# Kernel optimization log

Hardware: AMD Instinct MI355X
Metric: run time of the kernel (lower is better)

The kernel has to match this reference:

```python
import jax, jax.numpy as jnp
import numpy as np

LN_EPS = 1e-5
NORM_EPS = 1e-12


def entmax15_last(x):
    """Exact 1.5-entmax over the last axis (Peters & Martins sort algorithm)."""
    d = x.shape[-1]
    x = x / 2.0
    x = x - jnp.max(x, axis=-1, keepdims=True)
    xs = jnp.sort(x, axis=-1)[..., ::-1]  # descending
    k = jnp.arange(1, d + 1, dtype=x.dtype)
    mean = jnp.cumsum(xs, axis=-1) / k
    meansq = jnp.cumsum(xs * xs, axis=-1) / k
    ss = k * (meansq - jnp.square(mean))
    delta = (1.0 - ss) / k
    tau = mean - jnp.sqrt(jnp.clip(delta, 0.0))
    support = (tau <= xs).astype(jnp.int32)
    k_star = jnp.sum(support, axis=-1, keepdims=True) - 1  # last valid index
    tau_star = jnp.take_along_axis(tau, k_star, axis=-1)
    return jnp.square(jnp.maximum(x - tau_star, 0.0))


def layer_norm(x, gamma, beta):
    mu = jnp.mean(x, axis=-1, keepdims=True)
    var = jnp.mean(jnp.square(x - mu), axis=-1, keepdims=True)
    return (x - mu) / jnp.sqrt(var + LN_EPS) * gamma + beta


def setup_inputs() -> dict:
    key = jax.random.key(0)
    ks = jax.random.split(key, 4)
    B, M, N, D, T, L = 256, 64, 32, 128, 64, 128
    return {
        "x": jax.random.normal(ks[0], (B, M, D), dtype=jnp.float32),
        "route_weights": jax.random.normal(ks[1], (M, N, D, T), dtype=jnp.float32),
        "thread": jax.random.uniform(ks[2], (1, M, N), dtype=jnp.float32),
        "routing_leaves": jax.random.uniform(ks[3], (L, T), dtype=jnp.float32),
        "ln_gamma": jnp.ones((T,), dtype=jnp.float32),
        "ln_beta": jnp.zeros((T,), dtype=jnp.float32),
    }


def reference(x, route_weights, thread, routing_leaves, ln_gamma, ln_beta):
    # entmax15 over dim=-2 (the in_capsule_size axis D) of route_weights [M,N,D,T]
    w = jnp.swapaxes(route_weights, -1, -2)
    w = entmax15_last(w)
    weights = jnp.swapaxes(w, -1, -2)
    # priors: [B, M, N, T]
    priors = jnp.einsum('bmd,mndt->bmnt', x, weights)
    # routing
    leave_hash = routing_leaves / jnp.maximum(
        jnp.linalg.norm(routing_leaves, axis=-1, keepdims=True), NORM_EPS)
    votes = jax.nn.sigmoid(jnp.einsum('ld,bmnt->bmnl', leave_hash, priors)) if False else \
        jax.nn.sigmoid(jnp.einsum('ld,bmnd->bmnl', leave_hash, priors))  # [B,M,N,L]
    mean_cap = jnp.mean(votes, axis=1, keepdims=True)
    dis = jnp.mean(jnp.square(votes - mean_cap), axis=-1)  # [B,M,N]
    weight = jax.nn.relu(jnp.square(thread) - dis)
    prob = jax.nn.softmax(weight, axis=-2)  # over M (in capsules)
    next_caps = jnp.sum(prob[:, :, :, None] * priors, axis=1)  # [B,N,T]
    return layer_norm(next_caps, ln_gamma, ln_beta)
```

## Files before the change

### kernel.cpp

```cpp
#include <hip/hip_runtime.h>
#include <hip/hip_bf16.h>
#include <math.h>

#define B_ 256
#define M_ 64
#define N_ 32
#define D_ 128
#define T_ 64
#define L_ 128

typedef __attribute__((ext_vector_type(8))) short short8;
typedef __attribute__((ext_vector_type(4))) float floatx4;

__device__ __forceinline__ unsigned short f2bf(float f) {
  unsigned int u = __float_as_uint(f);
  unsigned int r = (u + 0x7fffu + ((u >> 16) & 1u)) >> 16;
  return (unsigned short)r;
}
__device__ __forceinline__ float bf2f(unsigned short s) {
  return __uint_as_float(((unsigned int)s) << 16);
}
__device__ __forceinline__ float frcp(float x) { return __builtin_amdgcn_rcpf(x); }

__global__ __launch_bounds__(256) void k_entmax(const float* __restrict__ rw,
                                                unsigned short* __restrict__ wq2,
                                                const float* __restrict__ x,
                                                const float* __restrict__ leaves,
                                                unsigned short* __restrict__ xb2,
                                                unsigned short* __restrict__ lhn,
                                                const float* __restrict__ thr,
                                                float* __restrict__ thrT) {
  const int tid = threadIdx.x;
  const int bx = blockIdx.x;
  if (bx >= 1024) {
    int bid = bx - 1024;
    if (bid < 512) {
      int idx = bid * 256 + tid;
      int j = idx & 7, b = (idx >> 3) & 255, m = idx >> 11;
      const float* xs = x + ((size_t)b * M_ + m) * D_ + j;
      unsigned short pv[16];
#pragma unroll
      for (int i = 0; i < 16; ++i) pv[i] = f2bf(xs[i * 8]);
      unsigned short* dst = xb2 + ((size_t)m * B_ + b) * D_ + j * 16;
      uint4 w0, w1;
      w0.x = pv[0] | ((unsigned)pv[1] << 16);  w0.y = pv[2] | ((unsigned)pv[3] << 16);
      w0.z = pv[4] | ((unsigned)pv[5] << 16);  w0.w = pv[6] | ((unsigned)pv[7] << 16);
      w1.x = pv[8] | ((unsigned)pv[9] << 16);  w1.y = pv[10] | ((unsigned)pv[11] << 16);
      w1.z = pv[12] | ((unsigned)pv[13] << 16); w1.w = pv[14] | ((unsigned)pv[15] << 16);
      *(uint4*)(dst) = w0;
      *(uint4*)(dst + 8) = w1;
    } else if (bid == 512) {
      if (tid < L_) {
        const float* r = leaves + tid * T_;
        float ss = 0.f;
        for (int i = 0; i < T_; ++i) ss = fmaf(r[i], r[i], ss);
        float inv = frcp(fmaxf(sqrtf(ss), 1e-12f));
        unsigned short* o = lhn + tid * T_;
        for (int i = 0; i < T_; ++i) o[i] = f2bf(r[i] * inv);
      }
    } else {
#pragma unroll
      for (int k = 0; k < 8; ++k) {
        int idx = k * 256 + tid;
        int nn = idx >> 6, mm = idx & 63;
        thrT[idx] = thr[mm * N_ + nn];
      }
    }
    return;
  }

  const int mn = bx * 2 + (tid >> 7);
  const int sub = tid & 127;
  const int g = sub >> 3;
  const int j = sub & 7;
  const float* base = rw + (size_t)mn * D_ * T_ + g * 4;

  floatx4 xv[16];
#pragma unroll
  for (int i = 0; i < 16; ++i)
    xv[i] = *(const floatx4*)(base + (size_t)(i * 8 + j) * T_);

  floatx4 mx = xv[0];
#pragma unroll
  for (int i = 1; i < 16; ++i)
#pragma unroll
    for (int c = 0; c < 4; ++c) mx[c] = fmaxf(mx[c], xv[i][c]);
#pragma unroll
  for (int off = 1; off <= 4; off <<= 1)
#pragma unroll
    for (int c = 0; c < 4; ++c) mx[c] = fmaxf(mx[c], __shfl_xor(mx[c], off));
#pragma unroll
  for (int i = 0; i < 16; ++i)
#pragma unroll
    for (int c = 0; c < 4; ++c) xv[i][c] = (xv[i][c] - mx[c]) * 0.5f;

  floatx4 lo = (floatx4){-1.f, -1.f, -1.f, -1.f};
  floatx4 hi = (floatx4){0.f, 0.f, 0.f, 0.f};
  for (int it = 0; it < 10; ++it) {
    floatx4 tau, f = (floatx4){0.f, 0.f, 0.f, 0.f};
#pragma unroll
    for (int c = 0; c < 4; ++c) tau[c] = 0.5f * (lo[c] + hi[c]);
#pragma unroll
    for (int i = 0; i < 16; ++i)
#pragma unroll
      for (int c = 0; c < 4; ++c) {
        float u = fmaxf(xv[i][c] - tau[c], 0.0f);
        f[c] = fmaf(u, u, f[c]);
      }
#pragma unroll
    for (int off = 1; off <= 4; off <<= 1)
#pragma unroll
      for (int c = 0; c < 4; ++c) f[c] += __shfl_xor(f[c], off);
#pragma unroll
    for (int c = 0; c < 4; ++c) {
      bool ge = f[c] >= 1.0f;
      lo[c] = ge ? tau[c] : lo[c];
      hi[c] = ge ? hi[c] : tau[c];
    }
  }
  floatx4 tau0, cnt = (floatx4){0,0,0,0}, s1 = (floatx4){0,0,0,0}, s2 = (floatx4){0,0,0,0};
#pragma unroll
  for (int c = 0; c < 4; ++c) tau0[c] = 0.5f * (lo[c] + hi[c]);
#pragma unroll
  for (int i = 0; i < 16; ++i)
#pragma unroll
    for (int c = 0; c < 4; ++c) {
      bool in = xv[i][c] > tau0[c];
      float q = in ? xv[i][c] : 0.0f;
      cnt[c] += in ? 1.0f : 0.0f;
      s1[c] += q;
      s2[c] = fmaf(q, q, s2[c]);
    }
#pragma unroll
  for (int off = 1; off <= 4; off <<= 1)
#pragma unroll
    for (int c = 0; c < 4; ++c) {
      cnt[c] += __shfl_xor(cnt[c], off);
      s1[c] += __shfl_xor(s1[c], off);
      s2[c] += __shfl_xor(s2[c], off);
    }
  floatx4 tau;
#pragma unroll
  for (int c = 0; c < 4; ++c) {
    float rc = frcp(cnt[c]);
    float mean = s1[c] * rc;
    float ss = s2[c] - mean * s1[c];
    float delta = (1.0f - ss) * rc;
    tau[c] = mean - sqrtf(fmaxf(delta, 0.0f));
  }

#pragma unroll
  for (int c = 0; c < 4; ++c) {
    unsigned short pv[16];
#pragma unroll
    for (int i = 0; i < 16; ++i) {
      float u = fmaxf(xv[i][c] - tau[c], 0.0f);
      pv[i] = f2bf(u * u);
    }
    unsigned short* dst = wq2 + ((size_t)mn * 64 + g * 4 + c) * D_ + j * 16;
    uint4 w0, w1;
    w0.x = pv[0] | ((unsigned)pv[1] << 16);  w0.y = pv[2] | ((unsigned)pv[3] << 16);
    w0.z = pv[4] | ((unsigned)pv[5] << 16);  w0.w = pv[6] | ((unsigned)pv[7] << 16);
    w1.x = pv[8] | ((unsigned)pv[9] << 16);  w1.y = pv[10] | ((unsigned)pv[11] << 16);
    w1.z = pv[12] | ((unsigned)pv[13] << 16); w1.w = pv[14] | ((unsigned)pv[15] << 16);
    *(uint4*)(dst) = w0;
    *(uint4*)(dst + 8) = w1;
  }
}

#define BS_STRIDE 136
__global__ __launch_bounds__(256, 4) void k_priors(const unsigned short* __restrict__ xb2,
                                                   const unsigned short* __restrict__ wq2,
                                                   unsigned short* __restrict__ priors) {
  const int n = blockIdx.x, m = blockIdx.y;
  const int tid = threadIdx.x;
  const int wid = tid >> 6, lane = tid & 63;
  const int row16 = lane & 15, quad = lane >> 4;
  __shared__ __align__(16) unsigned short Bs[64 * BS_STRIDE];
  __shared__ __align__(16) unsigned short Ct[128 * 72];

  short8 xfr[2][2][4];
#pragma unroll
  for (int c = 0; c < 2; ++c)
#pragma unroll
    for (int sub = 0; sub < 2; ++sub) {
      const int b = c * 128 + wid * 32 + sub * 16 + row16;
      const unsigned short* xptr = xb2 + ((size_t)m * B_ + b) * D_ + quad * 8;
#pragma unroll
      for (int ks = 0; ks < 4; ++ks) xfr[c][sub][ks] = *(const short8*)(xptr + ks * 32);
    }

  {
    const unsigned short* bsrc = wq2 + ((size_t)(m * N_ + n) * T_) * D_;
    int tr = tid >> 4, cc = tid & 15;
#pragma unroll
    for (int p = 0; p < 4; ++p) {
      int row = p * 16 + tr;
      uint4 v = *(const uint4*)(bsrc + row * D_ + cc * 8);
      *(uint4*)&Bs[row * BS_STRIDE + cc * 8] = v;
    }
  }
  __syncthreads();

#pragma unroll
  for (int c = 0; c < 2; ++c) {
    floatx4 acc[2][4];
#pragma unroll
    for (int sub = 0; sub < 2; ++sub)
#pragma unroll
      for (int cf = 0; cf < 4; ++cf) acc[sub][cf] = (floatx4){0.f, 0.f, 0.f, 0.f};

#pragma unroll
    for (int cf = 0; cf < 4; ++cf) {
      short8 afr[4];
#pragma unroll
      for (int ks = 0; ks < 4; ++ks)
        afr[ks] = *(const short8*)&Bs[(cf * 16 + row16) * BS_STRIDE + ks * 32 + quad * 8];
#pragma unroll
      for (int ks = 0; ks < 4; ++ks)
#pragma unroll
        for (int sub = 0; sub < 2; ++sub)
          acc[sub][cf] = __builtin_amdgcn_mfma_f32_16x16x32_bf16(afr[ks], xfr[c][sub][ks], acc[sub][cf], 0, 0, 0);
    }

    if (c) __syncthreads();
#pragma unroll
    for (int sub = 0; sub < 2; ++sub)
#pragma unroll
      for (int cf = 0; cf < 4; ++cf) {
        ushort4 o4;
        o4.x = f2bf(acc[sub][cf][0]); o4.y = f2bf(acc[sub][cf][1]);
        o4.z = f2bf(acc[sub][cf][2]); o4.w = f2bf(acc[sub][cf][3]);
        *(ushort4*)&Ct[(wid * 32 + sub * 16 + row16) * 72 + cf * 16 + quad * 4] = o4;
      }
    __syncthreads();

    {
      int q = tid >> 4, s = tid & 15;
      int row = q * 8 + (s >> 1);
      int half = s & 1;
      int b = c * 128 + row;
      const unsigned short* src = &Ct[row * 72 + half * 32];
      unsigned short* dst = priors + (((size_t)n * B_ + b) * M_ + m) * T_ + half * 32;
      uint4 a0 = *(const uint4*)(src);
      uint4 a1 = *(const uint4*)(src + 8);
      uint4 a2 = *(const uint4*)(src + 16);
      uint4 a3 = *(const uint4*)(src + 24);
      *(uint4*)(dst) = a0;
      *(uint4*)(dst + 8) = a1;
      *(uint4*)(dst + 16) = a2;
      *(uint4*)(dst + 24) = a3;
    }
  }
}

__global__ __launch_bounds__(256, 4) void k_route(const unsigned short* __restrict__ priors,
                                                  const unsigned short* __restrict__ lhn,
                                                  const float* __restrict__ thrT,
                                                  const float* __restrict__ gamma,
                                                  const float* __restrict__ beta,
                                                  float* __restrict__ out) {
  const int n = blockIdx.x, g4 = blockIdx.y;
  const int tid = threadIdx.x;
  const int wid = tid >> 6, lane = tid & 63;
  const int col = lane & 15, quad = lane >> 4;

  __shared__ float probL[4][64];

  const int b = g4 * 4 + wid;

  const unsigned short* base = priors + ((size_t)n * B_ + b) * (M_ * T_);
  short8 afr[4][2];
#pragma unroll
  for (int mt = 0; mt < 4; ++mt)
#pragma unroll
    for (int ks = 0; ks < 2; ++ks)
      afr[mt][ks] = *(const short8*)(base + (mt * 16 + col) * T_ + ks * 32 + quad * 8);

  float thv = thrT[n * 64 + lane];

  float dis[4][4];
#pragma unroll
  for (int mt = 0; mt < 4; ++mt)
#pragma unroll
    for (int r = 0; r < 4; ++r) dis[mt][r] = 0.f;

#pragma unroll
  for (int s4 = 0; s4 < 4; ++s4) {
    floatx4 acc[4][2];
#pragma unroll
    for (int mt = 0; mt < 4; ++mt)
#pragma unroll
      for (int lt = 0; lt < 2; ++lt) acc[mt][lt] = (floatx4){0.f, 0.f, 0.f, 0.f};

#pragma unroll
    for (int lt = 0; lt < 2; ++lt) {
#pragma unroll
      for (int ks = 0; ks < 2; ++ks) {
        short8 bfr = *(const short8*)(lhn + (s4 * 32 + lt * 16 + col) * T_ + ks * 32 + quad * 8);
#pragma unroll
        for (int mt = 0; mt < 4; ++mt)
          acc[mt][lt] = __builtin_amdgcn_mfma_f32_16x16x32_bf16(afr[mt][ks], bfr, acc[mt][lt], 0, 0, 0);
      }
    }

#pragma unroll
    for (int mt = 0; mt < 4; ++mt)
#pragma unroll
      for (int lt = 0; lt < 2; ++lt)
#pragma unroll
        for (int r = 0; r < 4; ++r)
          acc[mt][lt][r] = frcp(1.0f + __expf(-acc[mt][lt][r]));

    float mc[2];
#pragma unroll
    for (int lt = 0; lt < 2; ++lt) {
      float s = 0.f;
#pragma unroll
      for (int mt = 0; mt < 4; ++mt)
#pragma unroll
        for (int r = 0; r < 4; ++r) s += acc[mt][lt][r];
      s += __shfl_xor(s, 16);
      s += __shfl_xor(s, 32);
      mc[lt] = s * (1.0f / 64.0f);
    }

#pragma unroll
    for (int mt = 0; mt < 4; ++mt)
#pragma unroll
      for (int r = 0; r < 4; ++r) {
        float s = 0.f;
#pragma unroll
        for (int lt = 0; lt < 2; ++lt) {
          float df = acc[mt][lt][r] - mc[lt];
          s = fmaf(df, df, s);
        }
        dis[mt][r] += s;
      }
  }

#pragma unroll
  for (int off = 1; off <= 8; off <<= 1)
#pragma unroll
    for (int mt = 0; mt < 4; ++mt)
#pragma unroll
      for (int r = 0; r < 4; ++r) dis[mt][r] += __shfl_xor(dis[mt][r], off);

  float e[4][4];
  float mxw = 0.f;
#pragma unroll
  for (int mt = 0; mt < 4; ++mt)
#pragma unroll
    for (int r = 0; r < 4; ++r) {
      float th = __shfl(thv, mt * 16 + quad * 4 + r);
      float w = fmaxf(th * th - dis[mt][r] * (1.0f / 128.0f), 0.0f);
      e[mt][r] = w;
      mxw = fmaxf(mxw, w);
    }
  mxw = fmaxf(mxw, __shfl_xor(mxw, 16));
  mxw = fmaxf(mxw, __shfl_xor(mxw, 32));
  float ssum = 0.f;
#pragma unroll
  for (int mt = 0; mt < 4; ++mt)
#pragma unroll
    for (int r = 0; r < 4; ++r) {
      e[mt][r] = __expf(e[mt][r] - mxw);
      ssum += e[mt][r];
    }
  ssum += __shfl_xor(ssum, 16);
  ssum += __shfl_xor(ssum, 32);
  float inv = frcp(ssum);
  if (col == 0) {
#pragma unroll
    for (int mt = 0; mt < 4; ++mt)
#pragma unroll
      for (int r = 0; r < 4; ++r)
        probL[wid][mt * 16 + quad * 4 + r] = e[mt][r] * inv;
  }

  float pr[4];
#pragma unroll
  for (int mt = 0; mt < 4; ++mt) pr[mt] = probL[wid][mt * 16 + col];

  float o[2][8];
#pragma unroll
  for (int ks = 0; ks < 2; ++ks)
#pragma unroll
    for (int j = 0; j < 8; ++j) o[ks][j] = 0.f;
#pragma unroll
  for (int mt = 0; mt < 4; ++mt)
#pragma unroll
    for (int ks = 0; ks < 2; ++ks)
#pragma unroll
      for (int j = 0; j < 8; ++j)
        o[ks][j] = fmaf(pr[mt], bf2f((unsigned short)afr[mt][ks][j]), o[ks][j]);
#pragma unroll
  for (int off = 1; off <= 8; off <<= 1)
#pragma unroll
    for (int ks = 0; ks < 2; ++ks)
#pragma unroll
      for (int j = 0; j < 8; ++j) o[ks][j] += __shfl_xor(o[ks][j], off);

  float mu = 0.f;
#pragma unroll
  for (int ks = 0; ks < 2; ++ks)
#pragma unroll
    for (int j = 0; j < 8; ++j) mu += o[ks][j];
  mu += __shfl_xor(mu, 16);
  mu += __shfl_xor(mu, 32);
  mu *= (1.0f / 64.0f);
  float var = 0.f;
#pragma unroll
  for (int ks = 0; ks < 2; ++ks)
#pragma unroll
    for (int j = 0; j < 8; ++j) {
      float d = o[ks][j] - mu;
      o[ks][j] = d;
      var = fmaf(d, d, var);
    }
  var += __shfl_xor(var, 16);
  var += __shfl_xor(var, 32);
  var *= (1.0f / 64.0f);
  float rstd = rsqrtf(var + 1e-5f);

  if (col == 0) {
    float* obase = out + ((size_t)b * N_ + n) * T_;
#pragma unroll
    for (int ks = 0; ks < 2; ++ks) {
      int tb = ks * 32 + quad * 8;
      float4 g0 = *(const float4*)(gamma + tb);
      float4 g1 = *(const float4*)(gamma + tb + 4);
      float4 b0 = *(const float4*)(beta + tb);
      float4 b1 = *(const float4*)(beta + tb + 4);
      float4 r0, r1;
      r0.x = o[ks][0] * rstd * g0.x + b0.x;
      r0.y = o[ks][1] * rstd * g0.y + b0.y;
      r0.z = o[ks][2] * rstd * g0.z + b0.z;
      r0.w = o[ks][3] * rstd * g0.w + b0.w;
      r1.x = o[ks][4] * rstd * g1.x + b1.x;
      r1.y = o[ks][5] * rstd * g1.y + b1.y;
      r1.z = o[ks][6] * rstd * g1.z + b1.z;
      r1.w = o[ks][7] * rstd * g1.w + b1.w;
      *(float4*)(obase + tb) = r0;
      *(float4*)(obase + tb + 4) = r1;
    }
  }
}

extern "C" void kernel_launch(void* const* d_in, const int* in_sizes, int n_in,
                              void* d_out, int out_size, void* d_ws, size_t ws_size,
                              hipStream_t stream) {
  const float* x = (const float*)d_in[0];
  const float* rw = (const float*)d_in[1];
  const float* thr = (const float*)d_in[2];
  const float* leaves = (const float*)d_in[3];
  const float* gamma = (const float*)d_in[4];
  const float* beta = (const float*)d_in[5];
  float* out = (float*)d_out;

  char* ws = (char*)d_ws;
  unsigned short* wq2 = (unsigned short*)(ws);
  unsigned short* priors = (unsigned short*)(ws + 33554432);
  unsigned short* xb2 = (unsigned short*)(ws + 33554432 + 67108864);
  unsigned short* lhn = (unsigned short*)(ws + 100663296 + 4194304);
  float* thrT = (float*)(ws + 104857600 + 16384);

  hipLaunchKernelGGL(k_entmax, dim3(1538), dim3(256), 0, stream, rw, wq2, x, leaves, xb2, lhn, thr, thrT);
  hipLaunchKernelGGL(k_priors, dim3(32, 64), dim3(256), 0, stream, xb2, wq2, priors);
  hipLaunchKernelGGL(k_route, dim3(32, 64), dim3(256), 0, stream, priors, lhn, thrT, gamma, beta, out);
}
```

Before: 185.0 us.

## Fuse entmax weight computation into priors GEMM kernel, dropping bf16 weight buffer

```diff
diff --git a/kernel.cpp b/kernel.cpp
--- a/kernel.cpp
+++ b/kernel.cpp
@@ -22,162 +22,152 @@
 }
 __device__ __forceinline__ float frcp(float x) { return __builtin_amdgcn_rcpf(x); }
 
-__global__ __launch_bounds__(256) void k_entmax(const float* __restrict__ rw,
-                                                unsigned short* __restrict__ wq2,
-                                                const float* __restrict__ x,
-                                                const float* __restrict__ leaves,
-                                                unsigned short* __restrict__ xb2,
-                                                unsigned short* __restrict__ lhn,
-                                                const float* __restrict__ thr,
-                                                float* __restrict__ thrT) {
+__global__ __launch_bounds__(256) void k_prep(const float* __restrict__ x,
+                                              const float* __restrict__ leaves,
+                                              unsigned short* __restrict__ xb2,
+                                              unsigned short* __restrict__ lhn,
+                                              const float* __restrict__ thr,
+                                              float* __restrict__ thrT) {
   const int tid = threadIdx.x;
   const int bx = blockIdx.x;
-  if (bx >= 1024) {
-    int bid = bx - 1024;
-    if (bid < 512) {
-      int idx = bid * 256 + tid;
-      int j = idx & 7, b = (idx >> 3) & 255, m = idx >> 11;
-      const float* xs = x + ((size_t)b * M_ + m) * D_ + j;
-      unsigned short pv[16];
-#pragma unroll
-      for (int i = 0; i < 16; ++i) pv[i] = f2bf(xs[i * 8]);
-      unsigned short* dst = xb2 + ((size_t)m * B_ + b) * D_ + j * 16;
-      uint4 w0, w1;
-      w0.x = pv[0] | ((unsigned)pv[1] << 16);  w0.y = pv[2] | ((unsigned)pv[3] << 16);
-      w0.z = pv[4] | ((unsigned)pv[5] << 16);  w0.w = pv[6] | ((unsigned)pv[7] << 16);
-      w1.x = pv[8] | ((unsigned)pv[9] << 16);  w1.y = pv[10] | ((unsigned)pv[11] << 16);
-      w1.z = pv[12] | ((unsigned)pv[13] << 16); w1.w = pv[14] | ((unsigned)pv[15] << 16);
-      *(uint4*)(dst) = w0;
-      *(uint4*)(dst + 8) = w1;
-    } else if (bid == 512) {
-      if (tid < L_) {
-        const float* r = leaves + tid * T_;
-        float ss = 0.f;
-        for (int i = 0; i < T_; ++i) ss = fmaf(r[i], r[i], ss);
-        float inv = frcp(fmaxf(sqrtf(ss), 1e-12f));
-        unsigned short* o = lhn + tid * T_;
-        for (int i = 0; i < T_; ++i) o[i] = f2bf(r[i] * inv);
-      }
-    } else {
-#pragma unroll
-      for (int k = 0; k < 8; ++k) {
-        int idx = k * 256 + tid;
-        int nn = idx >> 6, mm = idx & 63;
-        thrT[idx] = thr[mm * N_ + nn];
-      }
-    }
-    return;
-  }
-
-  const int mn = bx * 2 + (tid >> 7);
-  const int sub = tid & 127;
-  const int g = sub >> 3;
-  const int j = sub & 7;
-  const float* base = rw + (size_t)mn * D_ * T_ + g * 4;
-
-  floatx4 xv[16];
-#pragma unroll
-  for (int i = 0; i < 16; ++i)
-    xv[i] = *(const floatx4*)(base + (size_t)(i * 8 + j) * T_);
-
-  floatx4 mx = xv[0];
-#pragma unroll
-  for (int i = 1; i < 16; ++i)
-#pragma unroll
-    for (int c = 0; c < 4; ++c) mx[c] = fmaxf(mx[c], xv[i][c]);
-#pragma unroll
-  for (int off = 1; off <= 4; off <<= 1)
-#pragma unroll
-    for (int c = 0; c < 4; ++c) mx[c] = fmaxf(mx[c], __shfl_xor(mx[c], off));
-#pragma unroll
-  for (int i = 0; i < 16; ++i)
-#pragma unroll
-    for (int c = 0; c < 4; ++c) xv[i][c] = (xv[i][c] - mx[c]) * 0.5f;
-
-  floatx4 lo = (floatx4){-1.f, -1.f, -1.f, -1.f};
-  floatx4 hi = (floatx4){0.f, 0.f, 0.f, 0.f};
-  for (int it = 0; it < 10; ++it) {
-    floatx4 tau, f = (floatx4){0.f, 0.f, 0.f, 0.f};
-#pragma unroll
-    for (int c = 0; c < 4; ++c) tau[c] = 0.5f * (lo[c] + hi[c]);
-#pragma unroll
-    for (int i = 0; i < 16; ++i)
-#pragma unroll
-      for (int c = 0; c < 4; ++c) {
-        float u = fmaxf(xv[i][c] - tau[c], 0.0f);
-        f[c] = fmaf(u, u, f[c]);
-      }
-#pragma unroll
-    for (int off = 1; off <= 4; off <<= 1)
-#pragma unroll
-      for (int c = 0; c < 4; ++c) f[c] += __shfl_xor(f[c], off);
-#pragma unroll
-    for (int c = 0; c < 4; ++c) {
-      bool ge = f[c] >= 1.0f;
-      lo[c] = ge ? tau[c] : lo[c];
-      hi[c] = ge ? hi[c] : tau[c];
-    }
-  }
-  floatx4 tau0, cnt = (floatx4){0,0,0,0}, s1 = (floatx4){0,0,0,0}, s2 = (floatx4){0,0,0,0};
-#pragma unroll
-  for (int c = 0; c < 4; ++c) tau0[c] = 0.5f * (lo[c] + hi[c]);
-#pragma unroll
-  for (int i = 0; i < 16; ++i)
-#pragma unroll
-    for (int c = 0; c < 4; ++c) {
-      bool in = xv[i][c] > tau0[c];
-      float q = in ? xv[i][c] : 0.0f;
-      cnt[c] += in ? 1.0f : 0.0f;
-      s1[c] += q;
-      s2[c] = fmaf(q, q, s2[c]);
-    }
-#pragma unroll
-  for (int off = 1; off <= 4; off <<= 1)
-#pragma unroll
-    for (int c = 0; c < 4; ++c) {
-      cnt[c] += __shfl_xor(cnt[c], off);
-      s1[c] += __shfl_xor(s1[c], off);
-      s2[c] += __shfl_xor(s2[c], off);
-    }
-  floatx4 tau;
-#pragma unroll
-  for (int c = 0; c < 4; ++c) {
-    float rc = frcp(cnt[c]);
-    float mean = s1[c] * rc;
-    float ss = s2[c] - mean * s1[c];
-    float delta = (1.0f - ss) * rc;
-    tau[c] = mean - sqrtf(fmaxf(delta, 0.0f));
-  }
-
-#pragma unroll
-  for (int c = 0; c < 4; ++c) {
-    unsigned short pv[16];
-#pragma unroll
-    for (int i = 0; i < 16; ++i) {
-      float u = fmaxf(xv[i][c] - tau[c], 0.0f);
-      pv[i] = f2bf(u * u);
-    }
-    unsigned short* dst = wq2 + ((size_t)mn * 64 + g * 4 + c) * D_ + j * 16;
-    uint4 w0, w1;
-    w0.x = pv[0] | ((unsigned)pv[1] << 16);  w0.y = pv[2] | ((unsigned)pv[3] << 16);
-    w0.z = pv[4] | ((unsigned)pv[5] << 16);  w0.w = pv[6] | ((unsigned)pv[7] << 16);
-    w1.x = pv[8] | ((unsigned)pv[9] << 16);  w1.y = pv[10] | ((unsigned)pv[11] << 16);
-    w1.z = pv[12] | ((unsigned)pv[13] << 16); w1.w = pv[14] | ((unsigned)pv[15] << 16);
-    *(uint4*)(dst) = w0;
-    *(uint4*)(dst + 8) = w1;
+  if (bx < 1024) {
+    int idx = bx * 256 + tid;
+    int j = idx & 15, b = (idx >> 4) & 255, m = idx >> 12;
+    const float* xs = x + ((size_t)b * M_ + m) * D_ + j;
+    unsigned short pv[8];
+#pragma unroll
+    for (int i = 0; i < 8; ++i) pv[i] = f2bf(xs[i * 16]);
+    unsigned short* dst = xb2 + ((size_t)m * B_ + b) * D_ + j * 8;
+    uint4 w;
+    w.x = pv[0] | ((unsigned)pv[1] << 16);
+    w.y = pv[2] | ((unsigned)pv[3] << 16);
+    w.z = pv[4] | ((unsigned)pv[5] << 16);
+    w.w = pv[6] | ((unsigned)pv[7] << 16);
+    *(uint4*)dst = w;
+  } else if (bx == 1024) {
+    if (tid < L_) {
+      const float* r = leaves + tid * T_;
+      float ss = 0.f;
+      for (int i = 0; i < T_; ++i) ss = fmaf(r[i], r[i], ss);
+      float inv = frcp(fmaxf(sqrtf(ss), 1e-12f));
+      unsigned short* o = lhn + tid * T_;
+      for (int i = 0; i < T_; ++i) o[i] = f2bf(r[i] * inv);
+    }
+  } else {
+#pragma unroll
+    for (int k = 0; k < 8; ++k) {
+      int idx = k * 256 + tid;
+      int nn = idx >> 6, mm = idx & 63;
+      thrT[idx] = thr[mm * N_ + nn];
+    }
   }
 }
 
 #define BS_STRIDE 136
-__global__ __launch_bounds__(256, 4) void k_priors(const unsigned short* __restrict__ xb2,
-                                                   const unsigned short* __restrict__ wq2,
-                                                   unsigned short* __restrict__ priors) {
-  const int n = blockIdx.x, m = blockIdx.y;
+__global__ __launch_bounds__(256, 4) void k_wpriors(const unsigned short* __restrict__ xb2,
+                                                    const float* __restrict__ rw,
+                                                    unsigned short* __restrict__ priors) {
+  const int m = blockIdx.x, n = blockIdx.y;
   const int tid = threadIdx.x;
   const int wid = tid >> 6, lane = tid & 63;
   const int row16 = lane & 15, quad = lane >> 4;
+
   __shared__ __align__(16) unsigned short Bs[64 * BS_STRIDE];
   __shared__ __align__(16) unsigned short Ct[128 * 72];
+
+  {
+    const int g = tid >> 4, j = tid & 15;
+    const float* base = rw + (size_t)(m * N_ + n) * (D_ * T_) + g * 4;
+    floatx4 xv[8];
+#pragma unroll
+    for (int i = 0; i < 8; ++i)
+      xv[i] = *(const floatx4*)(base + (size_t)(i * 16 + j) * T_);
+
+    floatx4 mx = xv[0];
+#pragma unroll
+    for (int i = 1; i < 8; ++i)
+#pragma unroll
+      for (int c = 0; c < 4; ++c) mx[c] = fmaxf(mx[c], xv[i][c]);
+#pragma unroll
+    for (int off = 1; off <= 8; off <<= 1)
+#pragma unroll
+      for (int c = 0; c < 4; ++c) mx[c] = fmaxf(mx[c], __shfl_xor(mx[c], off));
+#pragma unroll
+    for (int i = 0; i < 8; ++i)
+#pragma unroll
+      for (int c = 0; c < 4; ++c) xv[i][c] = (xv[i][c] - mx[c]) * 0.5f;
+
+    floatx4 lo = (floatx4){-1.f, -1.f, -1.f, -1.f};
+    floatx4 hi = (floatx4){0.f, 0.f, 0.f, 0.f};
+    for (int it = 0; it < 10; ++it) {
+      floatx4 tau, f = (floatx4){0.f, 0.f, 0.f, 0.f};
+#pragma unroll
+      for (int c = 0; c < 4; ++c) tau[c] = 0.5f * (lo[c] + hi[c]);
+#pragma unroll
+      for (int i = 0; i < 8; ++i)
+#pragma unroll
+        for (int c = 0; c < 4; ++c) {
+          float u = fmaxf(xv[i][c] - tau[c], 0.0f);
+          f[c] = fmaf(u, u, f[c]);
+        }
+#pragma unroll
+      for (int off = 1; off <= 8; off <<= 1)
+#pragma unroll
+        for (int c = 0; c < 4; ++c) f[c] += __shfl_xor(f[c], off);
+#pragma unroll
+      for (int c = 0; c < 4; ++c) {
+        bool ge = f[c] >= 1.0f;
+        lo[c] = ge ? tau[c] : lo[c];
+        hi[c] = ge ? hi[c] : tau[c];
+      }
+    }
+    floatx4 tau0, cnt = (floatx4){0,0,0,0}, s1 = (floatx4){0,0,0,0}, s2 = (floatx4){0,0,0,0};
+#pragma unroll
+    for (int c = 0; c < 4; ++c) tau0[c] = 0.5f * (lo[c] + hi[c]);
+#pragma unroll
+    for (int i = 0; i < 8; ++i)
+#pragma unroll
+      for (int c = 0; c < 4; ++c) {
+        bool in = xv[i][c] > tau0[c];
+        float q = in ? xv[i][c] : 0.0f;
+        cnt[c] += in ? 1.0f : 0.0f;
+        s1[c] += q;
+        s2[c] = fmaf(q, q, s2[c]);
+      }
+#pragma unroll
+    for (int off = 1; off <= 8; off <<= 1)
+#pragma unroll
+      for (int c = 0; c < 4; ++c) {
+        cnt[c] += __shfl_xor(cnt[c], off);
+        s1[c] += __shfl_xor(s1[c], off);
+        s2[c] += __shfl_xor(s2[c], off);
+      }
+    floatx4 tau;
+#pragma unroll
+    for (int c = 0; c < 4; ++c) {
+      float rc = frcp(cnt[c]);
+      float mean = s1[c] * rc;
+      float ss = s2[c] - mean * s1[c];
+      float delta = (1.0f - ss) * rc;
+      tau[c] = mean - sqrtf(fmaxf(delta, 0.0f));
+    }
+
+#pragma unroll
+    for (int c = 0; c < 4; ++c) {
+      unsigned short pv[8];
+#pragma unroll
+      for (int i = 0; i < 8; ++i) {
+        float u = fmaxf(xv[i][c] - tau[c], 0.0f);
+        pv[i] = f2bf(u * u);
+      }
+      uint4 w;
+      w.x = pv[0] | ((unsigned)pv[1] << 16);
+      w.y = pv[2] | ((unsigned)pv[3] << 16);
+      w.z = pv[4] | ((unsigned)pv[5] << 16);
+      w.w = pv[6] | ((unsigned)pv[7] << 16);
+      *(uint4*)&Bs[(g * 4 + c) * BS_STRIDE + j * 8] = w;
+    }
+  }
 
   short8 xfr[2][2][4];
 #pragma unroll
@@ -189,17 +179,6 @@
 #pragma unroll
       for (int ks = 0; ks < 4; ++ks) xfr[c][sub][ks] = *(const short8*)(xptr + ks * 32);
     }
-
-  {
-    const unsigned short* bsrc = wq2 + ((size_t)(m * N_ + n) * T_) * D_;
-    int tr = tid >> 4, cc = tid & 15;
-#pragma unroll
-    for (int p = 0; p < 4; ++p) {
-      int row = p * 16 + tr;
-      uint4 v = *(const uint4*)(bsrc + row * D_ + cc * 8);
-      *(uint4*)&Bs[row * BS_STRIDE + cc * 8] = v;
-    }
-  }
   __syncthreads();
 
 #pragma unroll
@@ -459,13 +438,12 @@
   float* out = (float*)d_out;
 
   char* ws = (char*)d_ws;
-  unsigned short* wq2 = (unsigned short*)(ws);
-  unsigned short* priors = (unsigned short*)(ws + 33554432);
-  unsigned short* xb2 = (unsigned short*)(ws + 33554432 + 67108864);
-  unsigned short* lhn = (unsigned short*)(ws + 100663296 + 4194304);
-  float* thrT = (float*)(ws + 104857600 + 16384);
-
-  hipLaunchKernelGGL(k_entmax, dim3(1538), dim3(256), 0, stream, rw, wq2, x, leaves, xb2, lhn, thr, thrT);
-  hipLaunchKernelGGL(k_priors, dim3(32, 64), dim3(256), 0, stream, xb2, wq2, priors);
+  unsigned short* priors = (unsigned short*)(ws);
+  unsigned short* xb2 = (unsigned short*)(ws + 67108864);
+  unsigned short* lhn = (unsigned short*)(ws + 71303168);
+  float* thrT = (float*)(ws + 71319552);
+
+  hipLaunchKernelGGL(k_prep, dim3(1026), dim3(256), 0, stream, x, leaves, xb2, lhn, thr, thrT);
+  hipLaunchKernelGGL(k_wpriors, dim3(64, 32), dim3(256), 0, stream, xb2, rw, priors);
   hipLaunchKernelGGL(k_route, dim3(32, 64), dim3(256), 0, stream, priors, lhn, thrT, gamma, beta, out);
 }
```

Measured after the change: 180.0 us. 1.03x faster.
